# Performance work log

Measured on AMD Instinct MI355X. Metric: run time of the kernel, lower is better.

Reference implementation:

```python
import jax, jax.numpy as jnp
import numpy as np


def setup_inputs() -> dict:
    key = jax.random.key(0)
    k1, k2 = jax.random.split(key)
    x = jax.random.normal(k1, (16, 1024, 512), dtype=jnp.float32)
    embedding = jax.random.normal(k2, (8192, 512), dtype=jnp.float32)
    return {"x": x, "embedding": embedding}


def reference(x, embedding):
    # x: [b, n, c], embedding (codebook k): [m, c]
    b, n, c = x.shape
    m = embedding.shape[0]
    q = x.reshape(b * n, c)            # (b n) c
    k = embedding
    # Squared L2 distance: ||q||^2 + ||k||^2 - 2 q.k  -> [bn, m]
    sim = (jnp.sum(q * q, axis=1, keepdims=True)
           + jnp.sum(k * k, axis=1)
           - 2.0 * jnp.einsum('nc,mc->nm', q, k))
    z_indices = jnp.argmin(sim, axis=1)                     # [bn]
    z_onehot = jax.nn.one_hot(z_indices, m, dtype=jnp.float32)  # [bn, m]
    # Direct gather is mathematically identical to onehot @ k
    z = k[z_indices]                                        # [bn, c]
    # Straight-through estimator: z = q + sg(z - q)
    z_st = q + jax.lax.stop_gradient(z - q)
    # Perplexity of code usage
    z_mean = jnp.mean(z_onehot, axis=0)                     # [m]
    perplexity = jnp.exp(-jnp.sum(z_mean * jnp.log(z_mean + 1e-10)))
    return (z_st.reshape(b, n, c),
            z_indices.reshape(b, n),
            z_onehot.reshape(b, n, m),
            perplexity)
```

## Files before the change

### kernel.cpp

```cpp
#include <hip/hip_runtime.h>
#include <cstdint>
#include <cstddef>

#define BNR 16384
#define C   512
#define M   8192
#define BM  128
#define BN  128
#define BK  64
#define NCH 8
#define NSETS 64

#define TILE_U16   8192
#define PANEL_U16  65536

typedef float f32x4 __attribute__((ext_vector_type(4)));
typedef _Float16 f16x8 __attribute__((ext_vector_type(8)));
typedef unsigned short u16;

static __device__ __forceinline__ u16 h_bits(_Float16 h) {
    union { _Float16 h; u16 u; } x; x.h = h; return x.u;
}
static __device__ __forceinline__ void gl_lds16(const void* g, void* l) {
    __builtin_amdgcn_global_load_lds(
        (const __attribute__((address_space(1))) void*)g,
        (__attribute__((address_space(3))) void*)l, 16, 0, 0);
}

__global__ void knorm_k(const float* __restrict__ emb, float* __restrict__ knorm) {
    int gw   = (blockIdx.x * blockDim.x + threadIdx.x) >> 6;
    int lane = threadIdx.x & 63;
    int nw   = (gridDim.x * blockDim.x) >> 6;
    for (int row = gw; row < M; row += nw) {
        const float4* p = (const float4*)(emb + (size_t)row * C);
        float s = 0.f;
#pragma unroll
        for (int j = 0; j < 2; ++j) {
            float4 v = p[lane + 64 * j];
            s += v.x * v.x + v.y * v.y + v.z * v.z + v.w * v.w;
        }
#pragma unroll
        for (int o = 32; o > 0; o >>= 1) s += __shfl_down(s, o, 64);
        if (lane == 0) knorm[row] = s;
    }
}

__global__ void cvt_tile_k(const float* __restrict__ in, u16* __restrict__ outp) {
    int o = blockIdx.x * 256 + threadIdx.x;
    int q = o & 1023, kb = q >> 7, row = q & 127;
    int c = (o >> 10) & 7, pan = o >> 13;
    int grow = pan * BM + row;
    int k0 = c * BK + kb * 8;
    const float4* src = (const float4*)(in + (size_t)grow * C + k0);
    float4 a = src[0], b = src[1];
    u16 v[8] = { h_bits((_Float16)a.x), h_bits((_Float16)a.y),
                 h_bits((_Float16)a.z), h_bits((_Float16)a.w),
                 h_bits((_Float16)b.x), h_bits((_Float16)b.y),
                 h_bits((_Float16)b.z), h_bits((_Float16)b.w) };
    u16* dst = outp + (size_t)o * 8;
    *(ushort4*)(dst)     = *(ushort4*)(v);
    *(ushort4*)(dst + 4) = *(ushort4*)(v + 4);
}

__global__ void mfma_argmin_k(
    const u16* __restrict__ x2t, const u16* __restrict__ e2t,
    const float* __restrict__ knorm,
    float* __restrict__ pv1, int* __restrict__ pi1,
    float* __restrict__ pv2, int* __restrict__ pi2) {
    __shared__ __align__(16) u16 ldsA[8][128][8];
    __shared__ __align__(16) u16 ldsB[8][128][8];

    const int tid  = threadIdx.x;
    const int lane = tid & 63;
    const int w    = tid >> 6;
    const int wm   = w >> 1, wn = w & 1;
    const int g    = lane >> 4, r = lane & 15;

    const int xk = blockIdx.x & 7, j = blockIdx.x >> 3;
    const int stid = (j >> 6) * 8 + xk;
    const int p  = j & 63;
    const int rb = (stid & 15) * 8 + (p & 7);
    const int cb = (stid >> 4) * 8 + (p >> 3);
    const int rowBase = rb * BM, colBase = cb * BN;

    f32x4 acc[4][4];
#pragma unroll
    for (int m = 0; m < 4; ++m)
#pragma unroll
        for (int n = 0; n < 4; ++n) acc[m][n] = (f32x4)(0.0f);

    const u16* aT = x2t + (size_t)rb * PANEL_U16;
    const u16* bT = e2t + (size_t)cb * PANEL_U16;

#pragma unroll 1
    for (int c = 0; c < NCH; ++c) {
        if (c) __syncthreads();
#pragma unroll
        for (int it = 0; it < 4; ++it) {
            int u = it * 256 + tid;
            gl_lds16(aT + (size_t)c * TILE_U16 + u * 8, (u16*)ldsA + u * 8);
            gl_lds16(bT + (size_t)c * TILE_U16 + u * 8, (u16*)ldsB + u * 8);
        }
        __syncthreads();

#pragma unroll
        for (int ks = 0; ks < 2; ++ks) {
            const int kb = ks * 4 + g;
            f16x8 a[4], b[4];
#pragma unroll
            for (int m = 0; m < 4; ++m)
                a[m] = *(const f16x8*)&ldsA[kb][wm * 64 + m * 16 + r][0];
#pragma unroll
            for (int n = 0; n < 4; ++n)
                b[n] = *(const f16x8*)&ldsB[kb][wn * 64 + n * 16 + r][0];
#pragma unroll
            for (int m = 0; m < 4; ++m)
#pragma unroll
                for (int n = 0; n < 4; ++n)
                    acc[m][n] = __builtin_amdgcn_mfma_f32_16x16x32_f16(
                        a[m], b[n], acc[m][n], 0, 0, 0);
        }
    }
    __syncthreads();

    float kn[4];
#pragma unroll
    for (int n = 0; n < 4; ++n) kn[n] = knorm[colBase + wn * 64 + n * 16 + r];

    float* mv = (float*)&ldsA[0][0][0];
    int*   mi = (int*)(mv + 2 * 128 * 2);

#pragma unroll
    for (int m = 0; m < 4; ++m) {
#pragma unroll
        for (int q = 0; q < 4; ++q) {
            float v1 = 3.0e38f, v2 = 3.0e38f;
            int   i1 = 0x7fffffff, i2 = 0x7fffffff;
#pragma unroll
            for (int n = 0; n < 4; ++n) {
                int col = colBase + wn * 64 + n * 16 + r;
                float d = fmaf(-2.0f, acc[m][n][q], kn[n]);
                if (d < v1 || (d == v1 && col < i1)) {
                    v2 = v1; i2 = i1; v1 = d; i1 = col;
                } else if (d < v2 || (d == v2 && col < i2)) {
                    v2 = d; i2 = col;
                }
            }
#pragma unroll
            for (int msk = 1; msk < 16; msk <<= 1) {
                float ov1 = __shfl_xor(v1, msk, 64);
                int   oi1 = __shfl_xor(i1, msk, 64);
                float ov2 = __shfl_xor(v2, msk, 64);
                int   oi2 = __shfl_xor(i2, msk, 64);
                bool ob = (ov1 < v1) || (ov1 == v1 && oi1 < i1);
                float nbv = ob ? ov1 : v1;  int nbi = ob ? oi1 : i1;
                float c1v = ob ? ov2 : v2;  int c1i = ob ? oi2 : i2;
                float c2v = ob ? v1 : ov1;  int c2i = ob ? i1 : oi1;
                bool cb2 = (c2v < c1v) || (c2v == c1v && c2i < c1i);
                v1 = nbv; i1 = nbi;
                v2 = cb2 ? c2v : c1v; i2 = cb2 ? c2i : c1i;
            }
            if (r == 0) {
                int lrow = wm * 64 + m * 16 + g * 4 + q;
                mv[(wn * 128 + lrow) * 2 + 0] = v1;
                mv[(wn * 128 + lrow) * 2 + 1] = v2;
                mi[(wn * 128 + lrow) * 2 + 0] = i1;
                mi[(wn * 128 + lrow) * 2 + 1] = i2;
            }
        }
    }
    __syncthreads();

    if (tid < 128) {
        float V1 = 3.0e38f, V2 = 3.0e38f;
        int   I1 = 0x7fffffff, I2 = 0x7fffffff;
#pragma unroll
        for (int s = 0; s < 4; ++s) {
            float d = mv[((s >> 1) * 128 + tid) * 2 + (s & 1)];
            int   ci = mi[((s >> 1) * 128 + tid) * 2 + (s & 1)];
            if (d < V1 || (d == V1 && ci < I1)) {
                V2 = V1; I2 = I1; V1 = d; I1 = ci;
            } else if (d < V2 || (d == V2 && ci < I2)) {
                V2 = d; I2 = ci;
            }
        }
        size_t o = (size_t)cb * BNR + rowBase + tid;
        pv1[o] = V1; pi1[o] = I1;
        pv2[o] = V2; pi2[o] = I2;
    }
}

__global__ void refine_k(const float* __restrict__ x, const float* __restrict__ emb,
                         const float* __restrict__ pv1, const int* __restrict__ pi1,
                         const float* __restrict__ pv2, const int* __restrict__ pi2,
                         float* __restrict__ out_idx) {
    int row  = blockIdx.x * 4 + (threadIdx.x >> 6);
    int lane = threadIdx.x & 63;
    size_t off = (size_t)lane * BNR + row;
    float va = pv1[off]; int ia = pi1[off];
    float vb = pv2[off]; int ib = pi2[off];
    int cand[8];
#pragma unroll
    for (int b = 0; b < 8; ++b) {
        bool al = (va < vb) || (va == vb && ia < ib);
        float cv = al ? va : vb; int ci = al ? ia : ib;
#pragma unroll
        for (int msk = 1; msk < 64; msk <<= 1) {
            float ov = __shfl_xor(cv, msk, 64);
            int   oi = __shfl_xor(ci, msk, 64);
            if (ov < cv || (ov == cv && oi < ci)) { cv = ov; ci = oi; }
        }
        cand[b] = ci;
        if (ia == ci) va = 3.0e38f;
        else if (ib == ci) vb = 3.0e38f;
    }
    int gid = lane >> 3, gl = lane & 7;
    int myc = cand[gid];
    const float* qp = x + (size_t)row * C;
    const float* kp = emb + (size_t)myc * C;
    double s = 0.0;
#pragma unroll 4
    for (int j = gl * 64; j < gl * 64 + 64; j += 4) {
        float4 q4 = *(const float4*)(qp + j);
        float4 k4 = *(const float4*)(kp + j);
        double d0 = (double)q4.x - (double)k4.x;
        double d1 = (double)q4.y - (double)k4.y;
        double d2 = (double)q4.z - (double)k4.z;
        double d3 = (double)q4.w - (double)k4.w;
        s += d0 * d0 + d1 * d1 + d2 * d2 + d3 * d3;
    }
    s += __shfl_xor(s, 1, 64);
    s += __shfl_xor(s, 2, 64);
    s += __shfl_xor(s, 4, 64);
    double dv = (gl == 0) ? s : 1.0e300;
    int    di = (gl == 0) ? myc : 0x7fffffff;
#pragma unroll
    for (int msk = 8; msk < 64; msk <<= 1) {
        double ov = __shfl_xor(dv, msk, 64);
        int    oi = __shfl_xor(di, msk, 64);
        if (ov < dv || (ov == dv && oi < di)) { dv = ov; di = oi; }
    }
    if (lane == 0) out_idx[row] = (float)di;
}

__global__ void gather_k(const float* __restrict__ emb, const float* __restrict__ out_idx,
                         float* __restrict__ zst, float* __restrict__ onehot) {
    int row = blockIdx.x;
    int idx = (int)out_idx[row];
    const float4* src = (const float4*)(emb + (size_t)idx * C);
    float4* dst = (float4*)(zst + (size_t)row * C);
    dst[threadIdx.x] = src[threadIdx.x];
    if (threadIdx.x == 0) onehot[(size_t)row * M + idx] = 1.0f;
}

__global__ void perp_k(const float* __restrict__ out_idx, float* __restrict__ out_perp) {
    __shared__ int hist[M];
    __shared__ float red[256];
    int tid = threadIdx.x;
    for (int j = tid; j < M; j += 256) hist[j] = 0;
    __syncthreads();
    for (int j = tid; j < BNR; j += 256) atomicAdd(&hist[(int)out_idx[j]], 1);
    __syncthreads();
    float s = 0.f;
    for (int j = tid; j < M; j += 256) {
        float pb = (float)hist[j] * (1.0f / (float)BNR);
        s += pb * logf(pb + 1e-10f);
    }
    red[tid] = s; __syncthreads();
    for (int o = 128; o > 0; o >>= 1) {
        if (tid < o) red[tid] += red[tid + o];
        __syncthreads();
    }
    if (tid == 0) out_perp[0] = expf(-red[0]);
}

extern "C" void kernel_launch(void* const* d_in, const int* in_sizes, int n_in,
                              void* d_out, int out_size, void* d_ws, size_t ws_size,
                              hipStream_t stream) {
    const float* x   = (const float*)d_in[0];
    const float* emb = (const float*)d_in[1];

    float* out        = (float*)d_out;
    float* out_zst    = out;
    float* out_idx    = out + (size_t)BNR * C;
    float* out_onehot = out_idx + BNR;
    float* out_perp   = out_onehot + (size_t)BNR * M;

    u16*   x2t   = (u16*)out_onehot;
    u16*   e2t   = x2t + (size_t)BNR * C;
    float* knorm = (float*)(e2t + (size_t)M * C);
    float* pv1   = knorm + M;
    float* pv2   = pv1 + (size_t)NSETS * BNR;
    int*   pi1   = (int*)(pv2 + (size_t)NSETS * BNR);
    int*   pi2   = pi1 + (size_t)NSETS * BNR;

    cvt_tile_k<<<(BNR * C / 8) / 256, 256, 0, stream>>>(x, x2t);
    cvt_tile_k<<<(M * C / 8) / 256, 256, 0, stream>>>(emb, e2t);
    knorm_k<<<64, 256, 0, stream>>>(emb, knorm);
    mfma_argmin_k<<<(BNR / BM) * (M / BN), 256, 0, stream>>>(
        x2t, e2t, knorm, pv1, pi1, pv2, pi2);
    refine_k<<<BNR / 4, 256, 0, stream>>>(x, emb, pv1, pi1, pv2, pi2, out_idx);

    hipMemsetAsync(out_onehot, 0, (size_t)BNR * M * sizeof(float), stream);
    gather_k<<<BNR, 128, 0, stream>>>(emb, out_idx, out_zst, out_onehot);
    perp_k<<<1, 256, 0, stream>>>(out_idx, out_perp);
}
```

Measured before the change: 480.4 us.

## Fuse one-hot zeroing into GEMM launch and move scratch to workspace

```diff
diff --git a/kernel.cpp b/kernel.cpp
--- a/kernel.cpp
+++ b/kernel.cpp
@@ -10,6 +10,10 @@
 #define BK  64
 #define NCH 8
 #define NSETS 64
+
+#define NZERO 512
+#define GEMM_BLOCKS 8192
+#define OH4_PER_ZB  65536
 
 #define TILE_U16   8192
 #define PANEL_U16  65536
@@ -62,21 +66,33 @@
     *(ushort4*)(dst + 4) = *(ushort4*)(v + 4);
 }
 
-__global__ void mfma_argmin_k(
+__global__ void mega_k(
     const u16* __restrict__ x2t, const u16* __restrict__ e2t,
     const float* __restrict__ knorm,
     float* __restrict__ pv1, int* __restrict__ pi1,
-    float* __restrict__ pv2, int* __restrict__ pi2) {
+    float* __restrict__ pv2, int* __restrict__ pi2,
+    float* __restrict__ onehot) {
     __shared__ __align__(16) u16 ldsA[8][128][8];
     __shared__ __align__(16) u16 ldsB[8][128][8];
 
+    if (blockIdx.x < NZERO) {
+        f32x4* o4 = (f32x4*)onehot;
+        size_t base = (size_t)blockIdx.x * OH4_PER_ZB + threadIdx.x;
+        const f32x4 z = (f32x4)(0.0f);
+#pragma unroll 4
+        for (int i = 0; i < OH4_PER_ZB / 256; ++i)
+            __builtin_nontemporal_store(z, &o4[base + (size_t)i * 256]);
+        return;
+    }
+
+    const int gid  = blockIdx.x - NZERO;
     const int tid  = threadIdx.x;
     const int lane = tid & 63;
     const int w    = tid >> 6;
     const int wm   = w >> 1, wn = w & 1;
     const int g    = lane >> 4, r = lane & 15;
 
-    const int xk = blockIdx.x & 7, j = blockIdx.x >> 3;
+    const int xk = gid & 7, j = gid >> 3;
     const int stid = (j >> 6) * 8 + xk;
     const int p  = j & 63;
     const int rb = (stid & 15) * 8 + (p & 7);
@@ -243,13 +259,14 @@
     if (lane == 0) out_idx[row] = (float)di;
 }
 
-__global__ void gather_k(const float* __restrict__ emb, const float* __restrict__ out_idx,
+__global__ void finish_k(const float* __restrict__ emb,
+                         const float* __restrict__ out_idx,
                          float* __restrict__ zst, float* __restrict__ onehot) {
     int row = blockIdx.x;
     int idx = (int)out_idx[row];
-    const float4* src = (const float4*)(emb + (size_t)idx * C);
-    float4* dst = (float4*)(zst + (size_t)row * C);
-    dst[threadIdx.x] = src[threadIdx.x];
+    const f32x4* src = (const f32x4*)(emb + (size_t)idx * C);
+    f32x4* dst = (f32x4*)(zst + (size_t)row * C);
+    __builtin_nontemporal_store(src[threadIdx.x], &dst[threadIdx.x]);
     if (threadIdx.x == 0) onehot[(size_t)row * M + idx] = 1.0f;
 }
 
@@ -286,7 +303,7 @@
     float* out_onehot = out_idx + BNR;
     float* out_perp   = out_onehot + (size_t)BNR * M;
 
-    u16*   x2t   = (u16*)out_onehot;
+    u16*   x2t   = (u16*)d_ws;
     u16*   e2t   = x2t + (size_t)BNR * C;
     float* knorm = (float*)(e2t + (size_t)M * C);
     float* pv1   = knorm + M;
@@ -297,11 +314,9 @@
     cvt_tile_k<<<(BNR * C / 8) / 256, 256, 0, stream>>>(x, x2t);
     cvt_tile_k<<<(M * C / 8) / 256, 256, 0, stream>>>(emb, e2t);
     knorm_k<<<64, 256, 0, stream>>>(emb, knorm);
-    mfma_argmin_k<<<(BNR / BM) * (M / BN), 256, 0, stream>>>(
-        x2t, e2t, knorm, pv1, pi1, pv2, pi2);
+    mega_k<<<NZERO + GEMM_BLOCKS, 256, 0, stream>>>(
+        x2t, e2t, knorm, pv1, pi1, pv2, pi2, out_onehot);
     refine_k<<<BNR / 4, 256, 0, stream>>>(x, emb, pv1, pi1, pv2, pi2, out_idx);
-
-    hipMemsetAsync(out_onehot, 0, (size_t)BNR * M * sizeof(float), stream);
-    gather_k<<<BNR, 128, 0, stream>>>(emb, out_idx, out_zst, out_onehot);
+    finish_k<<<BNR, 128, 0, stream>>>(emb, out_idx, out_zst, out_onehot);
     perp_k<<<1, 256, 0, stream>>>(out_idx, out_perp);
 }
```

New measurement: 465.9 us. 1.03x faster.
